# Kernel tuning notes

Hardware: AMD Instinct MI355X
Metric: run time of the kernel (lower is better)

Reference implementation:

```python
import jax, jax.numpy as jnp
import numpy as np
from jax import lax

B, C, H, W = 32, 256, 56, 56
NH, LC, DIL = 8, 7, 8  # heads, window size, dilation; H == LC*DIL -> exact dilated partition
N = LC * LC
DH = C // NH
SCALE = DH ** (-0.5)


def _rel_index():
    ch = np.arange(LC)
    coords = np.stack(np.meshgrid(ch, ch, indexing='ij')).reshape(2, -1)  # (2, 49)
    rel = (coords[:, :, None] - coords[:, None, :]).transpose(1, 2, 0)  # (49,49,2)
    rel[..., 0] += LC - 1
    rel[..., 1] += LC - 1
    rel[..., 0] *= 2 * LC - 1
    return jnp.asarray(rel.sum(-1))  # (49,49) int

REL_IDX = _rel_index()


def _layernorm(x, w, b, eps=1e-5):
    m = x.mean(-1, keepdims=True)
    v = ((x - m) ** 2).mean(-1, keepdims=True)
    return (x - m) * lax.rsqrt(v + eps) * w + b


def setup_inputs() -> dict:
    key = jax.random.key(0)
    ks = jax.random.split(key, 8)
    def n(k, shape, s=0.02):
        return jax.random.normal(k, shape, jnp.float32) * s
    return {
        'x': jax.random.normal(ks[0], (B, C, H, W), jnp.float32),
        'cpe_w': n(ks[1], (C, 1, 3, 3)),
        'cpe_b': jnp.zeros((C,), jnp.float32),
        'ln1_w': jnp.ones((C,), jnp.float32),
        'ln1_b': jnp.zeros((C,), jnp.float32),
        'rpb': n(ks[2], ((2 * LC - 1) ** 2, NH)),
        'qkv_w': n(ks[3], (C, 3 * C)),
        'qkv_b': jnp.zeros((3 * C,), jnp.float32),
        'proj_w': n(ks[4], (C, C)),
        'proj_b': jnp.zeros((C,), jnp.float32),
        'ln2_w': jnp.ones((C,), jnp.float32),
        'ln2_b': jnp.zeros((C,), jnp.float32),
        'fc1_w': n(ks[5], (C, 4 * C)),
        'fc1_b': jnp.zeros((4 * C,), jnp.float32),
        'fc2_w': n(ks[6], (4 * C, C)),
        'fc2_b': jnp.zeros((C,), jnp.float32),
    }


def reference(x, cpe_w, cpe_b, ln1_w, ln1_b, rpb, qkv_w, qkv_b, proj_w, proj_b,
              ln2_w, ln2_b, fc1_w, fc1_b, fc2_w, fc2_b):
    # CPE: depthwise 3x3 conv, residual
    cpe = lax.conv_general_dilated(x, cpe_w, (1, 1), 'SAME',
                                   dimension_numbers=('NCHW', 'OIHW', 'NCHW'),
                                   feature_group_count=C)
    x = x + cpe + cpe_b[None, :, None, None]
    x = x.transpose(0, 2, 3, 1)  # B,H,W,C
    shortcut = x
    xn = _layernorm(x, ln1_w, ln1_b)
    # dilated window partition (LD!=0): window (i,j) gathers pixels (i+DIL*t, j+DIL*u)
    xw = xn.reshape(B, LC, DIL, LC, DIL, C).transpose(0, 2, 4, 1, 3, 5)  # B,i,j,t,u,C
    x1 = xw.reshape(B * DIL * DIL, N, C)
    # window attention with relative position bias
    qkv = (x1 @ qkv_w + qkv_b).reshape(-1, N, 3, NH, DH).transpose(2, 0, 3, 1, 4)
    q, k, v = qkv[0] * SCALE, qkv[1], qkv[2]  # (Bn,NH,N,DH)
    attn = jnp.einsum('bhnd,bhmd->bhnm', q, k)
    bias = rpb[REL_IDX].transpose(2, 0, 1)  # (NH,N,N)
    attn = jax.nn.softmax(attn + bias[None], axis=-1)
    o = jnp.einsum('bhnm,bhmd->bhnd', attn, v).transpose(0, 2, 1, 3).reshape(-1, N, C)
    o = o @ proj_w + proj_b
    # scatter windows back to spatial positions (exact inverse of the partition)
    o = o.reshape(B, DIL, DIL, LC, LC, C).transpose(0, 3, 1, 4, 2, 5).reshape(B, H, W, C)
    x = shortcut + o
    h = _layernorm(x, ln2_w, ln2_b)
    h = jax.nn.gelu(h @ fc1_w + fc1_b, approximate=False) @ fc2_w + fc2_b
    x = x + h
    return x.transpose(0, 3, 1, 2)  # B,C,H,W
```

## Files before the change

kernel.cpp:

```cpp
#include <hip/hip_runtime.h>
#include <hip/hip_bf16.h>

#define DEVINL __device__ __forceinline__

constexpr int Cc  = 256;
constexpr int Hh  = 56;
constexpr int Ww  = 56;
constexpr int Tn  = 32 * 56 * 56;
constexpr int HW  = Hh * Ww;
constexpr float SCALEF = 0.17677669529663689f;

typedef __attribute__((ext_vector_type(4))) float f32x4;
typedef __attribute__((ext_vector_type(8))) short bf16x8;

DEVINL unsigned short f2bf(float f) {
  __hip_bfloat16 h = __float2bfloat16(f);
  return *reinterpret_cast<unsigned short*>(&h);
}
DEVINL float bf2f(unsigned short u) {
  union { unsigned int i; float f; } v; v.i = (unsigned int)u << 16; return v.f;
}

#define GLOAD_LDS16(gp, lp) \
  __builtin_amdgcn_global_load_lds((const __attribute__((address_space(1))) void*)(gp), \
                                   (__attribute__((address_space(3))) void*)(lp), 16, 0, 0)

__global__ __launch_bounds__(256) void cpe_kernel(const float* __restrict__ x,
    const float* __restrict__ cw, const float* __restrict__ cb,
    unsigned short* __restrict__ out)
{
  __shared__ unsigned short Xs[16 * 581];
  const int tid = threadIdx.x;
  const int bx  = blockIdx.x;
  const int cg  = bx & 15;
  const int t2  = bx >> 4;
  const int hg  = t2 % 7;
  const int b   = t2 / 7;
  const int c0  = cg * 16;
  const int h0  = hg * 8;

  for (int idx = tid; idx < 16 * 580; idx += 256) {
    const int ci  = idx / 580;
    const int rem = idx - ci * 580;
    const int rr  = rem / 58;
    const int wc  = rem - rr * 58;
    const int h2  = h0 - 1 + rr;
    const int w2  = wc - 1;
    float v = 0.f;
    if (h2 >= 0 && h2 < Hh && w2 >= 0 && w2 < Ww)
      v = x[((size_t)(b * Cc + c0 + ci)) * HW + h2 * Ww + w2];
    Xs[ci * 581 + rem] = f2bf(v);
  }
  __syncthreads();

  const int ci = tid & 15;
  const int c  = c0 + ci;
  float wr9[9];
  #pragma unroll
  for (int i = 0; i < 9; ++i) wr9[i] = cw[c * 9 + i];
  const float cbv = cb[c];
  const unsigned short* Xc = Xs + ci * 581;

  #pragma unroll
  for (int it = 0; it < 7; ++it) {
    const int tg   = it * 16 + (tid >> 4);
    const int tok0 = tg * 4;
    const int hr   = tok0 / 56;
    const int w0   = tok0 - hr * 56;
    float r0v[6], r1v[6], r2v[6];
    #pragma unroll
    for (int j = 0; j < 6; ++j) {
      r0v[j] = bf2f(Xc[hr * 58 + w0 + j]);
      r1v[j] = bf2f(Xc[(hr + 1) * 58 + w0 + j]);
      r2v[j] = bf2f(Xc[(hr + 2) * 58 + w0 + j]);
    }
    unsigned short ov[4];
    #pragma unroll
    for (int t = 0; t < 4; ++t) {
      float acc = r1v[t + 1];
      acc += wr9[0] * r0v[t] + wr9[1] * r0v[t + 1] + wr9[2] * r0v[t + 2];
      acc += wr9[3] * r1v[t] + wr9[4] * r1v[t + 1] + wr9[5] * r1v[t + 2];
      acc += wr9[6] * r2v[t] + wr9[7] * r2v[t + 1] + wr9[8] * r2v[t + 2];
      ov[t] = f2bf(acc + cbv);
    }
    const size_t tbase = (size_t)b * HW + (h0 + hr) * Ww + w0;
    #pragma unroll
    for (int t = 0; t < 4; ++t)
      out[(tbase + t) * Cc + c] = ov[t];
  }
}

__global__ __launch_bounds__(256) void stats_bf16(const unsigned short* __restrict__ in,
    float2* __restrict__ st)
{
  const int lane = threadIdx.x & 63;
  const size_t t = (size_t)blockIdx.x * 4 + (threadIdx.x >> 6);
  const ushort4 v = *reinterpret_cast<const ushort4*>(in + t * Cc + lane * 4);
  const float v0 = bf2f(v.x), v1 = bf2f(v.y), v2 = bf2f(v.z), v3 = bf2f(v.w);
  float s  = v0 + v1 + v2 + v3;
  float sq = v0 * v0 + v1 * v1 + v2 * v2 + v3 * v3;
  #pragma unroll
  for (int o = 32; o >= 1; o >>= 1) {
    s  += __shfl_xor(s, o);
    sq += __shfl_xor(sq, o);
  }
  if (lane == 0) {
    const float mean = s * (1.0f / Cc);
    const float var  = sq * (1.0f / Cc) - mean * mean;
    st[t] = make_float2(mean, rsqrtf(var + 1e-5f));
  }
}

__global__ __launch_bounds__(256) void ln_apply_bf16(const unsigned short* __restrict__ inp,
    const float* __restrict__ w, const float* __restrict__ b,
    unsigned short* __restrict__ out)
{
  const int lane = threadIdx.x & 63;
  const size_t t = (size_t)blockIdx.x * 4 + (threadIdx.x >> 6);
  const ushort4 v = *reinterpret_cast<const ushort4*>(inp + t * Cc + lane * 4);
  const float v0 = bf2f(v.x), v1 = bf2f(v.y), v2 = bf2f(v.z), v3 = bf2f(v.w);
  float s  = v0 + v1 + v2 + v3;
  float sq = v0 * v0 + v1 * v1 + v2 * v2 + v3 * v3;
  #pragma unroll
  for (int o = 32; o >= 1; o >>= 1) {
    s  += __shfl_xor(s, o);
    sq += __shfl_xor(sq, o);
  }
  const float mean = s * (1.0f / Cc);
  const float var  = sq * (1.0f / Cc) - mean * mean;
  const float r    = rsqrtf(var + 1e-5f);
  const float4 w4 = *reinterpret_cast<const float4*>(w + lane * 4);
  const float4 b4 = *reinterpret_cast<const float4*>(b + lane * 4);
  ushort4 o;
  o.x = f2bf((v0 - mean) * r * w4.x + b4.x);
  o.y = f2bf((v1 - mean) * r * w4.y + b4.y);
  o.z = f2bf((v2 - mean) * r * w4.z + b4.z);
  o.w = f2bf((v3 - mean) * r * w4.w + b4.w);
  *reinterpret_cast<ushort4*>(out + t * Cc + lane * 4) = o;
}

template<int QS>
__global__ __launch_bounds__(256) void wconv_kernel(const float* __restrict__ W,
    const float* __restrict__ g, unsigned short* __restrict__ Wt, int K, int N)
{
  __shared__ float Xs[32][33];
  const int kb = blockIdx.x * 32, nb = blockIdx.y * 32;
  const int tn = threadIdx.x & 31, tk = threadIdx.x >> 5;
  #pragma unroll
  for (int i = 0; i < 4; ++i) {
    const int k = kb + tk + i * 8;
    const float gv = g ? g[k] : 1.0f;
    Xs[tk + i * 8][tn] = W[(size_t)k * N + nb + tn] * gv;
  }
  __syncthreads();
  const int wk = threadIdx.x & 31, wn = threadIdx.x >> 5;
  #pragma unroll
  for (int i = 0; i < 4; ++i) {
    const int n = nb + wn + i * 8;
    const float s = (QS && n < 256) ? SCALEF : 1.0f;
    Wt[(size_t)n * K + kb + wk] = f2bf(Xs[wk][wn + i * 8] * s);
  }
}

template<int S>
__global__ __launch_bounds__(256) void colsum_kernel(const float* __restrict__ W,
    const float* __restrict__ g, const float* __restrict__ bvec,
    const float* __restrict__ bias, float* __restrict__ C1, float* __restrict__ CB,
    int K, int N)
{
  __shared__ float red[2][256];
  const int col = blockIdx.x * 64 + (threadIdx.x & 63);
  const int ks  = threadIdx.x >> 6;
  const int kq  = K >> 2;
  float a1 = 0.f, a2 = 0.f;
  for (int k = ks * kq; k < (ks + 1) * kq; ++k) {
    const float wv = W[(size_t)k * N + col];
    a1 += g[k] * wv;
    a2 += bvec[k] * wv;
  }
  red[0][threadIdx.x] = a1;
  red[1][threadIdx.x] = a2;
  __syncthreads();
  if (threadIdx.x < 64) {
    float s1 = 0.f, s2 = 0.f;
    #pragma unroll
    for (int i = 0; i < 4; ++i) { s1 += red[0][threadIdx.x + i * 64]; s2 += red[1][threadIdx.x + i * 64]; }
    const float sc = (S && col < 256) ? SCALEF : 1.0f;
    C1[col] = sc * s1;
    CB[col] = sc * (s2 + bias[col]);
  }
}

__global__ __launch_bounds__(256) void biasgen_kernel(const float* __restrict__ rpb,
    float* __restrict__ biasT)
{
  const int i = blockIdx.x * 256 + threadIdx.x;
  const int h = i >> 12, n = (i >> 6) & 63, m = i & 63;
  float v;
  if (m >= 49) {
    v = -1e30f;
  } else {
    const int nc = n < 49 ? n : 48;
    const int dI = nc / 7 - m / 7 + 6;
    const int dJ = nc % 7 - m % 7 + 6;
    v = rpb[(dI * 13 + dJ) * 8 + h];
  }
  biasT[i] = v;
}

template<int EPI, int OSW>
__global__ __launch_bounds__(256) void mfma_gemm(
    const unsigned short* __restrict__ A, const unsigned short* __restrict__ Bt,
    const float* __restrict__ bias, const float* __restrict__ C1,
    const float2* __restrict__ stats, const unsigned short* __restrict__ resp,
    void* __restrict__ outp, int K, int N, int row0, int n_outer, int n_inner)
{
  __shared__ unsigned short Asm[128 * 64];
  __shared__ unsigned short Bsm[128 * 64];
  const int tid  = threadIdx.x;
  const int lane = tid & 63;
  const int wid  = tid >> 6;
  const int wr   = wid >> 1;
  const int wc   = wid & 1;

  const int slot  = blockIdx.x >> 3;
  const int outer = (slot / n_inner) * 8 + (blockIdx.x & 7);
  const int inner = slot - (slot / n_inner) * n_inner;
  if (outer >= n_outer) return;
  const int bm = (OSW ? inner : outer) * 128;
  const int bn = (OSW ? outer : inner) * 128;

  f32x4 acc[4][4] = {};

  const int srow = (lane >> 3);
  const int skc  = ((lane & 7) ^ srow) * 8;

  for (int k0 = 0; k0 < K; k0 += 64) {
    #pragma unroll
    for (int i = 0; i < 4; ++i) {
      const int ch  = wid * 4 + i;
      const int row = ch * 8 + srow;
      GLOAD_LDS16(A  + (size_t)(bm + row) * K + k0 + skc, &Asm[ch * 512]);
      GLOAD_LDS16(Bt + (size_t)(bn + row) * K + k0 + skc, &Bsm[ch * 512]);
    }
    __syncthreads();

    const int xr = lane & 7;
    const int lg = lane >> 4;
    #pragma unroll
    for (int k32 = 0; k32 < 2; ++k32) {
      const int koff = ((k32 * 4 + lg) ^ xr) * 8;
      bf16x8 af[4], bv[4];
      #pragma unroll
      for (int f = 0; f < 4; ++f) {
        af[f] = *reinterpret_cast<const bf16x8*>(
            &Asm[(wr * 64 + f * 16 + (lane & 15)) * 64 + koff]);
        bv[f] = *reinterpret_cast<const bf16x8*>(
            &Bsm[(wc * 64 + f * 16 + (lane & 15)) * 64 + koff]);
      }
      #pragma unroll
      for (int fm = 0; fm < 4; ++fm)
        #pragma unroll
        for (int fn = 0; fn < 4; ++fn)
          acc[fm][fn] = __builtin_amdgcn_mfma_f32_16x16x32_bf16(
              af[fm], bv[fn], acc[fm][fn], 0, 0, 0);
    }
    __syncthreads();
  }

  const int lr4 = (lane >> 4) * 4;
  const int lc  = lane & 15;
  if constexpr (EPI == 0) {
    float rsv[4][4], rmv[4][4];
    #pragma unroll
    for (int fm = 0; fm < 4; ++fm)
      #pragma unroll
      for (int r = 0; r < 4; ++r) {
        const float2 st = stats[bm + wr * 64 + fm * 16 + lr4 + r];
        rsv[fm][r] = st.y;
        rmv[fm][r] = -st.y * st.x;
      }
    #pragma unroll
    for (int fn = 0; fn < 4; ++fn) {
      const int gcol = bn + wc * 64 + fn * 16 + lc;
      const float c1 = C1[gcol], cb = bias[gcol];
      #pragma unroll
      for (int fm = 0; fm < 4; ++fm)
        #pragma unroll
        for (int r = 0; r < 4; ++r) {
          const int grow = bm + wr * 64 + fm * 16 + lr4 + r;
          const float v = rsv[fm][r] * acc[fm][fn][r] + rmv[fm][r] * c1 + cb;
          ((unsigned short*)outp)[(size_t)grow * N + gcol] = f2bf(v);
        }
    }
  } else if constexpr (EPI == 4) {
    float bch[4][4];
    #pragma unroll
    for (int fm = 0; fm < 4; ++fm)
      #pragma unroll
      for (int r = 0; r < 4; ++r)
        bch[fm][r] = bias[bm + wr * 64 + fm * 16 + lr4 + r];
    #pragma unroll
    for (int fn = 0; fn < 4; ++fn) {
      const int gtok = bn + wc * 64 + fn * 16 + lc;
      const int mg = row0 + gtok;
      const int b  = mg / HW;
      const int sp = mg - b * HW;
      float* ob = (float*)outp + (size_t)b * 256 * HW + sp;
      #pragma unroll
      for (int fm = 0; fm < 4; ++fm)
        #pragma unroll
        for (int r = 0; r < 4; ++r) {
          const int ch = bm + wr * 64 + fm * 16 + lr4 + r;
          float v = acc[fm][fn][r] + bch[fm][r];
          v += bf2f(resp[(size_t)gtok * 256 + ch]);
          ob[(size_t)ch * HW] = v;
        }
    }
  } else {
    #pragma unroll
    for (int fn = 0; fn < 4; ++fn) {
      const int gcol = bn + wc * 64 + fn * 16 + lc;
      const float bvs = bias[gcol];
      #pragma unroll
      for (int fm = 0; fm < 4; ++fm) {
        #pragma unroll
        for (int r = 0; r < 4; ++r) {
          const int grow = bm + wr * 64 + fm * 16 + lr4 + r;
          float v = acc[fm][fn][r] + bvs;
          if constexpr (EPI == 1) {
            v += bf2f(resp[(size_t)grow * 256 + gcol]);
            ((unsigned short*)outp)[(size_t)grow * N + gcol] = f2bf(v);
          } else {
            const float z = 1.5957691f * (v + 0.044715f * v * v * v);
            v = v / (1.0f + __expf(-z));
            ((unsigned short*)outp)[(size_t)grow * N + gcol] = f2bf(v);
          }
        }
      }
    }
  }
}

__global__ __launch_bounds__(256) void attn_mfma(const unsigned short* __restrict__ qkv,
    const float* __restrict__ biasT, unsigned short* __restrict__ outD)
{
  __shared__ char smem[4 * 14848];
  const int tid  = threadIdx.x;
  const int lane = tid & 63;
  const int wid  = tid >> 6;
  char* base = smem + wid * 14848;
  char* Qs = base;
  char* Ks = base + 5120;
  char* Vt = base + 10240;
  char* Ps = base;

  const int blk = blockIdx.x;
  const int b   = blk >> 6;
  const int di  = (blk >> 3) & 7;
  const int dj  = blk & 7;
  const size_t t00 = (size_t)b * HW + di * Ww + dj;

  const int lg = lane >> 4;
  const int lc = lane & 15;

  for (int rep = 0; rep < 2; ++rep) {
    const int h = wid * 2 + rep;

    for (int i = lane; i < 300; i += 64) {
      if (i < 150) reinterpret_cast<unsigned long long*>(Qs + 49 * 80)[i] = 0ull;
      else         reinterpret_cast<unsigned long long*>(Ks + 49 * 80)[i - 150] = 0ull;
    }
    for (int i = lane; i < 192; i += 64) {
      const int row = i / 6, q = i - (i / 6) * 6;
      *reinterpret_cast<unsigned long long*>(Vt + row * 144 + 96 + q * 8) = 0ull;
    }

    for (int idx = lane; idx < 392; idx += 64) {
      const int row = idx >> 3, dq = idx & 7;
      const int li = row / 7, lj = row - (row / 7) * 7;
      const size_t t = t00 + (size_t)(li * 8) * Ww + lj * 8;
      const unsigned short* src = qkv + t * 768 + h * 32 + dq * 4;
      *reinterpret_cast<uint2*>(Qs + row * 80 + dq * 8) =
          *reinterpret_cast<const uint2*>(src);
      *reinterpret_cast<uint2*>(Ks + row * 80 + dq * 8) =
          *reinterpret_cast<const uint2*>(src + 256);
    }
    for (int idx = lane; idx < 784; idx += 64) {
      const int row = idx >> 4, q = idx & 15;
      const int li = row / 7, lj = row - (row / 7) * 7;
      const size_t t = t00 + (size_t)(li * 8) * Ww + lj * 8;
      const unsigned int v = *reinterpret_cast<const unsigned int*>(
          qkv + t * 768 + h * 32 + 512 + q * 2);
      *reinterpret_cast<unsigned short*>(Vt + (2 * q) * 144 + row * 2) =
          (unsigned short)(v & 0xffff);
      *reinterpret_cast<unsigned short*>(Vt + (2 * q + 1) * 144 + row * 2) =
          (unsigned short)(v >> 16);
    }

    f32x4 sacc[4][4] = {};
    {
      bf16x8 af[4], bv[4];
      #pragma unroll
      for (int f = 0; f < 4; ++f) {
        af[f] = *reinterpret_cast<const bf16x8*>(Qs + (f * 16 + lc) * 80 + lg * 16);
        bv[f] = *reinterpret_cast<const bf16x8*>(Ks + (f * 16 + lc) * 80 + lg * 16);
      }
      #pragma unroll
      for (int fm = 0; fm < 4; ++fm)
        #pragma unroll
        for (int fn = 0; fn < 4; ++fn)
          sacc[fm][fn] = __builtin_amdgcn_mfma_f32_16x16x32_bf16(
              af[fm], bv[fn], sacc[fm][fn], 0, 0, 0);
    }

    const float* bh = biasT + h * 4096;
    #pragma unroll
    for (int fm = 0; fm < 4; ++fm) {
      float rowv[4][4];
      #pragma unroll
      for (int r = 0; r < 4; ++r) {
        const int n = fm * 16 + lg * 4 + r;
        #pragma unroll
        for (int fn = 0; fn < 4; ++fn)
          rowv[r][fn] = sacc[fm][fn][r] + bh[n * 64 + fn * 16 + lc];
      }
      #pragma unroll
      for (int r = 0; r < 4; ++r) {
        float mx = fmaxf(fmaxf(rowv[r][0], rowv[r][1]), fmaxf(rowv[r][2], rowv[r][3]));
        #pragma unroll
        for (int o = 8; o >= 1; o >>= 1) mx = fmaxf(mx, __shfl_xor(mx, o));
        float p[4], sm = 0.f;
        #pragma unroll
        for (int fn = 0; fn < 4; ++fn) { p[fn] = __expf(rowv[r][fn] - mx); sm += p[fn]; }
        #pragma unroll
        for (int o = 8; o >= 1; o >>= 1) sm += __shfl_xor(sm, o);
        const float inv = 1.0f / sm;
        const int n = fm * 16 + lg * 4 + r;
        #pragma unroll
        for (int fn = 0; fn < 4; ++fn)
          *reinterpret_cast<unsigned short*>(Ps + n * 144 + (fn * 16 + lc) * 2) =
              f2bf(p[fn] * inv);
      }
    }

    f32x4 oacc[4][2] = {};
    #pragma unroll
    for (int ks = 0; ks < 2; ++ks) {
      bf16x8 pa[4], vb[2];
      #pragma unroll
      for (int fm = 0; fm < 4; ++fm)
        pa[fm] = *reinterpret_cast<const bf16x8*>(
            Ps + (fm * 16 + lc) * 144 + ks * 64 + lg * 16);
      #pragma unroll
      for (int fn = 0; fn < 2; ++fn)
        vb[fn] = *reinterpret_cast<const bf16x8*>(
            Vt + (fn * 16 + lc) * 144 + ks * 64 + lg * 16);
      #pragma unroll
      for (int fm = 0; fm < 4; ++fm)
        #pragma unroll
        for (int fn = 0; fn < 2; ++fn)
          oacc[fm][fn] = __builtin_amdgcn_mfma_f32_16x16x32_bf16(
              pa[fm], vb[fn], oacc[fm][fn], 0, 0, 0);
    }

    #pragma unroll
    for (int fm = 0; fm < 4; ++fm) {
      #pragma unroll
      for (int r = 0; r < 4; ++r) {
        const int n = fm * 16 + lg * 4 + r;
        if (n < 49) {
          const int li = n / 7, lj = n - (n / 7) * 7;
          const size_t t = t00 + (size_t)(li * 8) * Ww + lj * 8;
          outD[t * 256 + h * 32 + lc]      = f2bf(oacc[fm][0][r]);
          outD[t * 256 + h * 32 + 16 + lc] = f2bf(oacc[fm][1][r]);
        }
      }
    }
  }
}

extern "C" void kernel_launch(void* const* d_in, const int* in_sizes, int n_in,
                              void* d_out, int out_size, void* d_ws, size_t ws_size,
                              hipStream_t stream) {
  (void)in_sizes; (void)n_in; (void)out_size;
  const float* x      = (const float*)d_in[0];
  const float* cpe_w  = (const float*)d_in[1];
  const float* cpe_b  = (const float*)d_in[2];
  const float* ln1_w  = (const float*)d_in[3];
  const float* ln1_b  = (const float*)d_in[4];
  const float* rpb    = (const float*)d_in[5];
  const float* qkv_w  = (const float*)d_in[6];
  const float* qkv_b  = (const float*)d_in[7];
  const float* proj_w = (const float*)d_in[8];
  const float* proj_b = (const float*)d_in[9];
  const float* ln2_w  = (const float*)d_in[10];
  const float* ln2_b  = (const float*)d_in[11];
  const float* fc1_w  = (const float*)d_in[12];
  const float* fc1_b  = (const float*)d_in[13];
  const float* fc2_w  = (const float*)d_in[14];
  const float* fc2_b  = (const float*)d_in[15];

  char* ws = (char*)d_ws;
  unsigned short* qkv_wt  = (unsigned short*)(ws);
  unsigned short* proj_wt = (unsigned short*)(ws + 393216);
  unsigned short* fc1_wt  = (unsigned short*)(ws + 524288);
  unsigned short* fc2_wt  = (unsigned short*)(ws + 1048576);
  float*  C1q = (float*)(ws + 1572864);
  float*  CBq = (float*)(ws + 1575936);

  const int NB_rt = (ws_size >= 157000000ull) ? 16 : 8;
  const int MCHrt = NB_rt * HW;
  const int NCH   = 32 / NB_rt;
  const int NOUT  = MCHrt / 128;

  unsigned short *slotX, *slotQ, *slotE;
  float2* statsFull = nullptr;
  float*  biasTp;
  if (NB_rt == 8) {
    slotX  = (unsigned short*)(ws + 1579008);
    slotQ  = (unsigned short*)(ws + 14424064);
    slotE  = (unsigned short*)(ws + 65804288);
    biasTp = (float*)(ws + 65804288 + 200704);
  } else {
    biasTp    = (float*)(ws + 1579008);
    statsFull = (float2*)(ws + 1710080);
    size_t o = 2512896;
    slotX = (unsigned short*)(ws + o); o += (size_t)MCHrt * 256 * 2;
    slotQ = (unsigned short*)(ws + o); o += (size_t)MCHrt * 768 * 2;
    slotE = (unsigned short*)(ws + o);
  }

  unsigned short* Araw = (unsigned short*)d_out + 25690112;

  wconv_kernel<1><<<dim3(8, 24), 256, 0, stream>>>(qkv_w,  ln1_w,  qkv_wt,  256, 768);
  wconv_kernel<0><<<dim3(8, 8),  256, 0, stream>>>(proj_w, nullptr, proj_wt, 256, 256);
  wconv_kernel<0><<<dim3(8, 32), 256, 0, stream>>>(fc1_w,  nullptr, fc1_wt,  256, 1024);
  wconv_kernel<0><<<dim3(32, 8), 256, 0, stream>>>(fc2_w,  nullptr, fc2_wt,  1024, 256);
  colsum_kernel<1><<<12, 256, 0, stream>>>(qkv_w, ln1_w, ln1_b, qkv_b, C1q, CBq, 256, 768);

  cpe_kernel<<<32 * 7 * 16, 256, 0, stream>>>(x, cpe_w, cpe_b, Araw);

  if (NB_rt != 8) {
    stats_bf16<<<Tn / 4, 256, 0, stream>>>(Araw, statsFull);
    biasgen_kernel<<<128, 256, 0, stream>>>(rpb, biasTp);
  }

  for (int c = 0; c < NCH; ++c) {
    const int r0 = c * MCHrt;
    const unsigned short* Ac = Araw + (size_t)r0 * Cc;
    const float2* stp;
    if (NB_rt == 8) {
      float2* stloc = (float2*)slotE;
      stats_bf16<<<MCHrt / 4, 256, 0, stream>>>(Ac, stloc);
      biasgen_kernel<<<128, 256, 0, stream>>>(rpb, biasTp);
      stp = stloc;
    } else {
      stp = statsFull + r0;
    }
    mfma_gemm<0, 0><<<NOUT * 6, 256, 0, stream>>>(
        Ac, qkv_wt, CBq, C1q, stp, nullptr, slotQ, 256, 768, 0, NOUT, 6);
    attn_mfma<<<NB_rt * 64, 256, 0, stream>>>(slotQ, biasTp, slotX);
    mfma_gemm<1, 0><<<NOUT * 2, 256, 0, stream>>>(
        slotX, proj_wt, proj_b, nullptr, nullptr, Ac, slotE, 256, 256, 0, NOUT, 2);
    ln_apply_bf16<<<MCHrt / 4, 256, 0, stream>>>(slotE, ln2_w, ln2_b, slotX);

    if (NB_rt == 8) {
      mfma_gemm<2, 0><<<((NOUT + 7) & ~7) * 8, 256, 0, stream>>>(
          slotX, fc1_wt, fc1_b, nullptr, nullptr, nullptr, slotQ, 256, 1024, 0, NOUT, 8);
      mfma_gemm<4, 1><<<((NOUT + 7) & ~7) * 2, 256, 0, stream>>>(
          fc2_wt, slotQ, fc2_b, nullptr, nullptr, slotE, d_out, 1024, 256, r0, NOUT, 2);
    } else {
      const int HTOK = MCHrt / 2;
      const int NOH  = HTOK / 128;
      const int NOHP = (NOH + 7) & ~7;
      for (int half = 0; half < 2; ++half) {
        const int off = half * HTOK;
        mfma_gemm<2, 0><<<NOHP * 8, 256, 0, stream>>>(
            slotX + (size_t)off * 256, fc1_wt, fc1_b, nullptr, nullptr, nullptr,
            slotQ, 256, 1024, 0, NOH, 8);
        mfma_gemm<4, 1><<<NOHP * 2, 256, 0, stream>>>(
            fc2_wt, slotQ, fc2_b, nullptr, nullptr, slotE + (size_t)off * 256,
            d_out, 1024, 256, r0 + off, NOH, 2);
      }
    }
  }
}
```

Before: 679.9 us.

## Fuse MLP fc1+GELU+fc2 into one kernel and process whole batch per chunk

Adds a fused MLP kernel that computes fc1, GELU and fc2 per 128-token tile, keeping the 1024-wide hidden activation in LDS so it never round-trips through global memory. The chunk size grows to the full batch of 32 when the workspace is large enough, which removes the split into halves and cuts launches. The CPE conv LDS rows are padded to 60 elements so rows can be read with vector loads. The cost is heavy LDS use (about 80KB) and a long serial hidden loop per block, which may limit occupancy. If the workspace is smaller than the new threshold, it falls back to the 8-image path.

```diff
diff --git a/kernel.cpp b/kernel.cpp
--- a/kernel.cpp
+++ b/kernel.cpp
@@ -20,6 +20,10 @@
 DEVINL float bf2f(unsigned short u) {
   union { unsigned int i; float f; } v; v.i = (unsigned int)u << 16; return v.f;
 }
+DEVINL float gelu_fast(float v) {
+  const float z = 1.5957691f * (v + 0.044715f * v * v * v);
+  return v / (1.0f + __expf(-z));
+}
 
 #define GLOAD_LDS16(gp, lp) \
   __builtin_amdgcn_global_load_lds((const __attribute__((address_space(1))) void*)(gp), \
@@ -29,7 +33,7 @@
     const float* __restrict__ cw, const float* __restrict__ cb,
     unsigned short* __restrict__ out)
 {
-  __shared__ unsigned short Xs[16 * 581];
+  __shared__ unsigned short Xs[16 * 620];
   const int tid = threadIdx.x;
   const int bx  = blockIdx.x;
   const int cg  = bx & 15;
@@ -49,7 +53,7 @@
     float v = 0.f;
     if (h2 >= 0 && h2 < Hh && w2 >= 0 && w2 < Ww)
       v = x[((size_t)(b * Cc + c0 + ci)) * HW + h2 * Ww + w2];
-    Xs[ci * 581 + rem] = f2bf(v);
+    Xs[ci * 620 + rr * 60 + wc] = f2bf(v);
   }
   __syncthreads();
 
@@ -59,7 +63,7 @@
   #pragma unroll
   for (int i = 0; i < 9; ++i) wr9[i] = cw[c * 9 + i];
   const float cbv = cb[c];
-  const unsigned short* Xc = Xs + ci * 581;
+  const unsigned short* Xc = Xs + ci * 620;
 
   #pragma unroll
   for (int it = 0; it < 7; ++it) {
@@ -67,20 +71,21 @@
     const int tok0 = tg * 4;
     const int hr   = tok0 / 56;
     const int w0   = tok0 - hr * 56;
-    float r0v[6], r1v[6], r2v[6];
-    #pragma unroll
-    for (int j = 0; j < 6; ++j) {
-      r0v[j] = bf2f(Xc[hr * 58 + w0 + j]);
-      r1v[j] = bf2f(Xc[(hr + 1) * 58 + w0 + j]);
-      r2v[j] = bf2f(Xc[(hr + 2) * 58 + w0 + j]);
+    float rv[3][6];
+    #pragma unroll
+    for (int j = 0; j < 3; ++j) {
+      const ushort4 a = *reinterpret_cast<const ushort4*>(Xc + (hr + j) * 60 + w0);
+      const ushort2 e = *reinterpret_cast<const ushort2*>(Xc + (hr + j) * 60 + w0 + 4);
+      rv[j][0] = bf2f(a.x); rv[j][1] = bf2f(a.y); rv[j][2] = bf2f(a.z);
+      rv[j][3] = bf2f(a.w); rv[j][4] = bf2f(e.x); rv[j][5] = bf2f(e.y);
     }
     unsigned short ov[4];
     #pragma unroll
     for (int t = 0; t < 4; ++t) {
-      float acc = r1v[t + 1];
-      acc += wr9[0] * r0v[t] + wr9[1] * r0v[t + 1] + wr9[2] * r0v[t + 2];
-      acc += wr9[3] * r1v[t] + wr9[4] * r1v[t + 1] + wr9[5] * r1v[t + 2];
-      acc += wr9[6] * r2v[t] + wr9[7] * r2v[t + 1] + wr9[8] * r2v[t + 2];
+      float acc = rv[1][t + 1];
+      acc += wr9[0] * rv[0][t] + wr9[1] * rv[0][t + 1] + wr9[2] * rv[0][t + 2];
+      acc += wr9[3] * rv[1][t] + wr9[4] * rv[1][t + 1] + wr9[5] * rv[1][t + 2];
+      acc += wr9[6] * rv[2][t] + wr9[7] * rv[2][t + 1] + wr9[8] * rv[2][t + 2];
       ov[t] = f2bf(acc + cbv);
     }
     const size_t tbase = (size_t)b * HW + (h0 + hr) * Ww + w0;
@@ -332,13 +337,154 @@
             v += bf2f(resp[(size_t)grow * 256 + gcol]);
             ((unsigned short*)outp)[(size_t)grow * N + gcol] = f2bf(v);
           } else {
-            const float z = 1.5957691f * (v + 0.044715f * v * v * v);
-            v = v / (1.0f + __expf(-z));
+            v = gelu_fast(v);
             ((unsigned short*)outp)[(size_t)grow * N + gcol] = f2bf(v);
           }
         }
       }
     }
+  }
+}
+
+__global__ __launch_bounds__(512) void mlp_fused(
+    const unsigned short* __restrict__ G,
+    const unsigned short* __restrict__ W1t,
+    const unsigned short* __restrict__ W2t,
+    const float* __restrict__ b1,
+    const float* __restrict__ b2,
+    const unsigned short* __restrict__ E,
+    float* __restrict__ outp, int row0)
+{
+  __shared__ unsigned short Gs[128 * 64];
+  __shared__ unsigned short Wsb[256 * 64];
+  __shared__ unsigned short Hs[128 * 128];
+  const int tid  = threadIdx.x;
+  const int lane = tid & 63;
+  const int wid  = tid >> 6;
+  const int bm   = blockIdx.x * 128;
+
+  const int w1r = wid >> 1;
+  const int w1c = wid & 1;
+  const int w2c = wid >> 1;
+  const int w2t = wid & 1;
+
+  const int srow = lane >> 3;
+  const int skc  = ((lane & 7) ^ srow) * 8;
+  const int lc   = lane & 15;
+  const int lg   = lane >> 4;
+  const int xr   = lane & 7;
+
+  f32x4 oacc[4][4] = {};
+
+  for (int s = 0; s < 8; ++s) {
+    const int h0 = s * 128;
+    f32x4 hacc[2][4] = {};
+
+    for (int k0 = 0; k0 < 256; k0 += 64) {
+      #pragma unroll
+      for (int i = 0; i < 4; ++i) {
+        const int ch = wid * 4 + i;
+        if (ch < 16) {
+          const int row = ch * 8 + srow;
+          GLOAD_LDS16(G + (size_t)(bm + row) * 256 + k0 + skc, &Gs[ch * 512]);
+        } else {
+          const int row = (ch - 16) * 8 + srow;
+          GLOAD_LDS16(W1t + (size_t)(h0 + row) * 256 + k0 + skc, &Wsb[(ch - 16) * 512]);
+        }
+      }
+      __syncthreads();
+      #pragma unroll
+      for (int k32 = 0; k32 < 2; ++k32) {
+        const int koff = ((k32 * 4 + lg) ^ xr) * 8;
+        bf16x8 af[2], bv[4];
+        #pragma unroll
+        for (int f = 0; f < 2; ++f)
+          af[f] = *reinterpret_cast<const bf16x8*>(
+              &Gs[(w1r * 32 + f * 16 + lc) * 64 + koff]);
+        #pragma unroll
+        for (int f = 0; f < 4; ++f)
+          bv[f] = *reinterpret_cast<const bf16x8*>(
+              &Wsb[(w1c * 64 + f * 16 + lc) * 64 + koff]);
+        #pragma unroll
+        for (int fm = 0; fm < 2; ++fm)
+          #pragma unroll
+          for (int fn = 0; fn < 4; ++fn)
+            hacc[fm][fn] = __builtin_amdgcn_mfma_f32_16x16x32_bf16(
+                af[fm], bv[fn], hacc[fm][fn], 0, 0, 0);
+      }
+      __syncthreads();
+    }
+
+    #pragma unroll
+    for (int fn = 0; fn < 4; ++fn) {
+      const int col = w1c * 64 + fn * 16 + lc;
+      const float bb = b1[h0 + col];
+      const int kg = col >> 6, cw = (col >> 3) & 7, ce = col & 7;
+      #pragma unroll
+      for (int fm = 0; fm < 2; ++fm)
+        #pragma unroll
+        for (int r = 0; r < 4; ++r) {
+          const int row = w1r * 32 + fm * 16 + lg * 4 + r;
+          const float v = gelu_fast(hacc[fm][fn][r] + bb);
+          Hs[row * 128 + kg * 64 + ((cw ^ (row & 7)) << 3) + ce] = f2bf(v);
+        }
+    }
+
+    #pragma unroll
+    for (int k20 = 0; k20 < 128; k20 += 64) {
+      #pragma unroll
+      for (int i = 0; i < 4; ++i) {
+        const int ch  = wid * 4 + i;
+        const int row = ch * 8 + srow;
+        GLOAD_LDS16(W2t + (size_t)row * 1024 + h0 + k20 + skc, &Wsb[ch * 512]);
+      }
+      __syncthreads();
+      #pragma unroll
+      for (int k32 = 0; k32 < 2; ++k32) {
+        const int koff = ((k32 * 4 + lg) ^ xr) * 8;
+        bf16x8 af[4], bv[4];
+        #pragma unroll
+        for (int f = 0; f < 4; ++f)
+          af[f] = *reinterpret_cast<const bf16x8*>(
+              &Wsb[(w2c * 64 + f * 16 + lc) * 64 + koff]);
+        #pragma unroll
+        for (int f = 0; f < 4; ++f)
+          bv[f] = *reinterpret_cast<const bf16x8*>(
+              &Hs[(w2t * 64 + f * 16 + lc) * 128 + k20 + koff]);
+        #pragma unroll
+        for (int fm = 0; fm < 4; ++fm)
+          #pragma unroll
+          for (int fn = 0; fn < 4; ++fn)
+            oacc[fm][fn] = __builtin_amdgcn_mfma_f32_16x16x32_bf16(
+                af[fm], bv[fn], oacc[fm][fn], 0, 0, 0);
+      }
+      __syncthreads();
+    }
+  }
+
+  const int lr4 = lg * 4;
+  float bch[4][4];
+  #pragma unroll
+  for (int fm = 0; fm < 4; ++fm)
+    #pragma unroll
+    for (int r = 0; r < 4; ++r)
+      bch[fm][r] = b2[w2c * 64 + fm * 16 + lr4 + r];
+  #pragma unroll
+  for (int fn = 0; fn < 4; ++fn) {
+    const int gtok = bm + w2t * 64 + fn * 16 + lc;
+    const int mg = row0 + gtok;
+    const int b  = mg / HW;
+    const int sp = mg - b * HW;
+    float* ob = outp + (size_t)b * 256 * HW + sp;
+    #pragma unroll
+    for (int fm = 0; fm < 4; ++fm)
+      #pragma unroll
+      for (int r = 0; r < 4; ++r) {
+        const int ch = w2c * 64 + fm * 16 + lr4 + r;
+        float v = oacc[fm][fn][r] + bch[fm][r];
+        v += bf2f(E[(size_t)gtok * 256 + ch]);
+        ob[(size_t)ch * HW] = v;
+      }
   }
 }
 
@@ -509,7 +655,7 @@
   float*  C1q = (float*)(ws + 1572864);
   float*  CBq = (float*)(ws + 1575936);
 
-  const int NB_rt = (ws_size >= 157000000ull) ? 16 : 8;
+  const int NB_rt = (ws_size >= 260000000ull) ? 32 : 8;
   const int MCHrt = NB_rt * HW;
   const int NCH   = 32 / NB_rt;
   const int NOUT  = MCHrt / 128;
@@ -571,18 +717,8 @@
       mfma_gemm<4, 1><<<((NOUT + 7) & ~7) * 2, 256, 0, stream>>>(
           fc2_wt, slotQ, fc2_b, nullptr, nullptr, slotE, d_out, 1024, 256, r0, NOUT, 2);
     } else {
-      const int HTOK = MCHrt / 2;
-      const int NOH  = HTOK / 128;
-      const int NOHP = (NOH + 7) & ~7;
-      for (int half = 0; half < 2; ++half) {
-        const int off = half * HTOK;
-        mfma_gemm<2, 0><<<NOHP * 8, 256, 0, stream>>>(
-            slotX + (size_t)off * 256, fc1_wt, fc1_b, nullptr, nullptr, nullptr,
-            slotQ, 256, 1024, 0, NOH, 8);
-        mfma_gemm<4, 1><<<NOHP * 2, 256, 0, stream>>>(
-            fc2_wt, slotQ, fc2_b, nullptr, nullptr, slotE + (size_t)off * 256,
-            d_out, 1024, 256, r0 + off, NOH, 2);
-      }
-    }
-  }
-}
+      mlp_fused<<<MCHrt / 128, 512, 0, stream>>>(
+          slotX, fc1_wt, fc2_wt, fc1_b, fc2_b, slotE, (float*)d_out, r0);
+    }
+  }
+}
```

Measured after the change: 707.1 us. 4.0% more time.
